# Kernel tuning notes

Measured on AMD Instinct MI355X. Metric: run time of the kernel, lower is better.

Reference implementation:

```python
import jax, jax.numpy as jnp
import numpy as np

BETA = 0.5      # conf.beta (undefined global in original repo)
ALPHA = 0.2     # LeakyReLU negative slope (init arg alpha)
N, E, FIN, FOUT = 50000, 1_600_000, 128, 64


def setup_inputs() -> dict:
    key = jax.random.key(0)
    k1, k2, k3, k4, k5 = jax.random.split(key, 5)
    inp = jax.random.normal(k1, (N, FIN), dtype=jnp.float32)
    edge = jax.random.randint(k2, (2, E), 0, N)                      # [2,E] (src,dst), = adj.nonzero().t()
    M_vals = jax.random.uniform(k3, (E,), dtype=jnp.float32)          # M gathered at edges
    # xavier_normal with gain 1.414, matching torch init
    W = jax.random.normal(k4, (FIN, FOUT), dtype=jnp.float32) * (1.414 * np.sqrt(2.0 / (FIN + FOUT)))
    a = jax.random.normal(k5, (2 * FOUT,), dtype=jnp.float32) * (1.414 * np.sqrt(2.0 / (1 + 2 * FOUT)))
    return {"input": inp, "M_vals": M_vals, "W": W, "a": a, "edge": edge}


def reference(input, M_vals, W, a, edge):
    n, f = input.shape[0], W.shape[1]
    src, dst = edge[0], edge[1]
    h = input @ W                                   # [N, F]
    # M = beta*M + (1-beta)*adj; at edges adj == 1
    bias = M_vals * BETA + (1.0 - BETA)             # [E]
    # a . cat(h_src, bias*h_dst) == (h@a[:F])[src] + bias * (h@a[F:])[dst]
    s1 = h @ a[:f]                                  # [N]
    s2 = h @ a[f:]                                  # [N]
    edge_e = jnp.exp(jax.nn.leaky_relu(s1[src] + bias * s2[dst], negative_slope=ALPHA))  # [E]
    # special_spmm(edge, e, [N,N], ones) -> per-row sum of edge weights
    e_rowsum = jax.ops.segment_sum(edge_e, src, num_segments=n)       # [N]
    # special_spmm(edge, e, [N,N], h) -> weighted aggregation of dst features into src rows
    h_prime = jax.ops.segment_sum(edge_e[:, None] * h[dst], src, num_segments=n)  # [N, F]
    h_prime = h_prime / e_rowsum[:, None]
    return jax.nn.elu(h_prime)                      # concat=True
```

## Files before the change

### kernel.cpp

```cpp
#include <hip/hip_runtime.h>
#include <hip/hip_bf16.h>

#define NN   50000
#define EE   1600000
#define FIN  128
#define FOUT 64
#define BETA  0.5f
#define ALPHA 0.2f
#define SBW    256
#define NB2    196
#define RCAP   9000
#define PGRID  400
#define PCHUNK 4000
#define CAP3   9008
#define XS     136

typedef __attribute__((ext_vector_type(8))) short short8;
typedef __attribute__((ext_vector_type(8))) unsigned short ushort8v;
typedef __attribute__((ext_vector_type(4))) float float4v;

__device__ __forceinline__ float load_any(const void* p, long i, int isf32) {
    if (isf32) return ((const float*)p)[i];
    unsigned int b = ((unsigned int)(((const unsigned short*)p)[i])) << 16;
    return __uint_as_float(b);
}

__device__ __forceinline__ unsigned short f32_to_bf16_rne(float f) {
    unsigned int b = __float_as_uint(f);
    return (unsigned short)((b + 0x7FFF + ((b >> 16) & 1)) >> 16);
}

__device__ __forceinline__ float bf16_to_f32(unsigned short u) {
    return __uint_as_float(((unsigned int)u) << 16);
}

__global__ __launch_bounds__(256) void detwt_kernel(
    const void* __restrict__ W, const void* __restrict__ Mv,
    unsigned short* __restrict__ Wt, int* __restrict__ flags,
    int* __restrict__ bcur)
{
    __shared__ int vote;
    const int tid = threadIdx.x;
    if (tid == 0) vote = 0;
    __syncthreads();

    int m = 0;
    const float vw = bf16_to_f32(((const unsigned short*)W)[tid * 16]);
    if (isnan(vw) || fabsf(vw) > 1e4f) m |= 1;
    if (blockIdx.x == 0) {
        const long half = (long)EE >> 1;
        const long pos = 2 * (((long)tid * (half / 256)) % half);
        const float vm = bf16_to_f32(((const unsigned short*)Mv)[pos]);
        if (isnan(vm) || fabsf(vm) > 1e4f) m |= 2;
    }
    if (m) atomicOr(&vote, m);
    __syncthreads();

    const int fW = vote & 1;
    if (blockIdx.x == 0) {
        if (tid == 0) flags[1] = (vote >> 1) & 1;
        if (tid < NB2) bcur[tid] = 0;
    }
    const int i = blockIdx.x * 256 + tid;
    const int k = i >> 6, n = i & 63;
    Wt[n * FIN + k] = f32_to_bf16_rne(load_any(W, i, fW));
}

__global__ __launch_bounds__(256) void mfma_gemm_kernel(
    const void* __restrict__ inp,
    const unsigned short* __restrict__ Wt,
    const void* __restrict__ a,
    unsigned short* __restrict__ h,
    float* __restrict__ s1,
    float* __restrict__ s2,
    int* __restrict__ flags)
{
    __shared__ unsigned short Xs[16 * XS];
    __shared__ float part1[4][16];
    __shared__ float part2[4][16];
    __shared__ int vote;

    const int tid  = threadIdx.x;
    const int wave = tid >> 6;
    const int lane = tid & 63;
    const int quad = lane >> 4;
    const int col  = lane & 15;
    const int rb   = blockIdx.x * 16;

    if (tid == 0) vote = 0;
    __syncthreads();

    {
        int m = 0;
        const float vi = bf16_to_f32(((const unsigned short*)inp)[(long)rb * FIN + tid * 8]);
        if (isnan(vi) || fabsf(vi) > 1e4f) m |= 1;
        if (tid < 128) {
            const float va = bf16_to_f32(((const unsigned short*)a)[tid]);
            if (isnan(va) || fabsf(va) > 1e4f) m |= 2;
        }
        if (m) atomicOr(&vote, m);
    }
    __syncthreads();
    const int fI = vote & 1, fA = (vote >> 1) & 1;
    if (blockIdx.x == 0 && tid == 0) flags[0] = fI;

    {
        const int r = tid >> 4, k8 = (tid & 15) * 8;
        if (!fI) {
            const unsigned short* src = (const unsigned short*)inp + (long)(rb + r) * FIN + k8;
            *(ushort8v*)&Xs[r * XS + k8] = *(const ushort8v*)src;
        } else {
            const float* src = (const float*)inp + (long)(rb + r) * FIN + k8;
            ushort8v v;
            #pragma unroll
            for (int j = 0; j < 8; ++j) v[j] = f32_to_bf16_rne(src[j]);
            *(ushort8v*)&Xs[r * XS + k8] = v;
        }
    }
    __syncthreads();

    const int nb = wave * 16;
    float4v acc = { 0.f, 0.f, 0.f, 0.f };
    #pragma unroll
    for (int k0 = 0; k0 < FIN; k0 += 32) {
        const short8 af = *(const short8*)&Xs[col * XS + k0 + quad * 8];
        const short8 bf = *(const short8*)&Wt[(long)(nb + col) * FIN + k0 + quad * 8];
        acc = __builtin_amdgcn_mfma_f32_16x16x32_bf16(af, bf, acc, 0, 0, 0);
    }

    #pragma unroll
    for (int r = 0; r < 4; ++r)
        h[(long)(rb + quad * 4 + r) * FOUT + nb + col] = f32_to_bf16_rne(acc[r]);

    const float a1 = load_any(a, nb + col, fA);
    const float a2 = load_any(a, 64 + nb + col, fA);
    #pragma unroll
    for (int r = 0; r < 4; ++r) {
        float v1 = acc[r] * a1;
        float v2 = acc[r] * a2;
        #pragma unroll
        for (int o = 1; o < 16; o <<= 1) {
            v1 += __shfl_xor(v1, o, 64);
            v2 += __shfl_xor(v2, o, 64);
        }
        if (col == 0) {
            part1[wave][quad * 4 + r] = v1;
            part2[wave][quad * 4 + r] = v2;
        }
    }
    __syncthreads();
    if (tid < 16) {
        s1[rb + tid] = part1[0][tid] + part1[1][tid] + part1[2][tid] + part1[3][tid];
        s2[rb + tid] = part2[0][tid] + part2[1][tid] + part2[2][tid] + part2[3][tid];
    }
}

__global__ __launch_bounds__(1024) void partition_kernel(
    const int* __restrict__ edge,
    const void* __restrict__ Mv,
    const int* __restrict__ flags,
    const float* __restrict__ s1,
    const float* __restrict__ s2,
    int* __restrict__ bcur,
    unsigned long long* __restrict__ recs)
{
    __shared__ int lcnt[NB2];
    __shared__ int lbase[NB2];
    const int tid = threadIdx.x;
    const int fM = flags[1];
    const int e0 = blockIdx.x * PCHUNK;

    if (tid < NB2) lcnt[tid] = 0;
    __syncthreads();

    int srcs[4], dsts[4];
    float mvs[4];
    #pragma unroll
    for (int k = 0; k < 4; ++k) {
        const int e = e0 + tid + 1024 * k;
        const bool ok = (tid + 1024 * k) < PCHUNK;
        srcs[k] = ok ? edge[e] : -1;
        dsts[k] = ok ? edge[EE + e] : 0;
        mvs[k]  = ok ? load_any(Mv, e, fM) : 0.f;
    }
    #pragma unroll
    for (int k = 0; k < 4; ++k)
        if (srcs[k] >= 0) atomicAdd(&lcnt[srcs[k] >> 8], 1);
    __syncthreads();

    if (tid < NB2) {
        const int c = lcnt[tid];
        const int o = c ? atomicAdd(&bcur[tid], c) : 0;
        lbase[tid] = tid * RCAP + o;
        lcnt[tid] = 0;
    }
    __syncthreads();

    float ss1[4], ss2[4];
    #pragma unroll
    for (int k = 0; k < 4; ++k) {
        ss1[k] = (srcs[k] >= 0) ? s1[srcs[k]] : 0.f;
        ss2[k] = (srcs[k] >= 0) ? s2[dsts[k]] : 0.f;
    }
    #pragma unroll
    for (int k = 0; k < 4; ++k) {
        if (srcs[k] < 0) continue;
        const float bias = mvs[k] * BETA + (1.f - BETA);
        const float x  = ss1[k] + bias * ss2[k];
        const float lr = x > 0.f ? x : ALPHA * x;
        const float ee = __expf(lr);
        const int b = srcs[k] >> 8;
        const int r = atomicAdd(&lcnt[b], 1);
        const int pos = lbase[b] + r;
        if (pos < (b + 1) * RCAP)
            recs[pos] = ((unsigned long long)(unsigned)srcs[k] << 32)
                      | ((unsigned long long)(unsigned)dsts[k] << 16)
                      | (unsigned long long)f32_to_bf16_rne(ee);
    }
}

__global__ __launch_bounds__(1024) void csr_spmm_kernel(
    const int* __restrict__ bcur,
    const unsigned long long* __restrict__ recs,
    const unsigned short* __restrict__ h,
    const int* __restrict__ flags,
    void* __restrict__ out)
{
    __shared__ unsigned long long lrec[CAP3];
    __shared__ unsigned int lpair[CAP3];
    __shared__ int cnt[SBW];
    __shared__ int off[SBW];
    __shared__ int wsum[4];
    const int b    = blockIdx.x;
    const int tid  = threadIdx.x;
    const int rb   = b * SBW;
    const int beg  = b * RCAP;

    int n = bcur[b]; if (n > RCAP) n = RCAP;

    if (tid < SBW) cnt[tid] = 0;
    __syncthreads();

    for (int j = tid; j < n; j += 1024) {
        const unsigned long long rec = recs[beg + j];
        const int r = (int)(rec >> 32) - rb;
        const int rank = atomicAdd(&cnt[r], 1);
        lrec[j] = ((unsigned long long)(unsigned)(r | (rank << 8)) << 32)
                | (unsigned long long)(unsigned)(rec & 0xFFFFFFFFu);
    }
    __syncthreads();

    int c = 0, x = 0;
    if (tid < SBW) {
        const int lane = tid & 63;
        c = cnt[tid];
        x = c;
        #pragma unroll
        for (int o = 1; o < 64; o <<= 1) {
            int y = __shfl_up(x, o, 64);
            if (lane >= o) x += y;
        }
        if (lane == 63) wsum[tid >> 6] = x;
    }
    __syncthreads();
    if (tid < SBW) {
        const int wv = tid >> 6;
        int wb = 0;
        for (int w = 0; w < wv; ++w) wb += wsum[w];
        off[tid] = wb + x - c;
    }
    __syncthreads();

    for (int j = tid; j < n; j += 1024) {
        const unsigned long long rec = lrec[j];
        const unsigned int hi = (unsigned int)(rec >> 32);
        lpair[off[hi & 255u] + (hi >> 8)] = (unsigned int)(rec & 0xFFFFFFFFu);
    }
    __syncthreads();

    const int wv   = tid >> 6;
    const int lane = tid & 63;
    const int g    = lane >> 3;
    const int sl   = lane & 7;
    const int fOut = flags[0];

    for (int rr = wv; rr < SBW; rr += 16) {
        const int row = rb + rr;
        if (row >= NN) break;
        const int jb = off[rr];
        const int je = jb + cnt[rr];

        float acc0 = 0.f, acc1 = 0.f, acc2 = 0.f, acc3 = 0.f;
        float acc4 = 0.f, acc5 = 0.f, acc6 = 0.f, acc7 = 0.f;
        float rsum = 0.f;
        int j = jb;
        for (; j + 31 < je; j += 32) {
            unsigned int u[4];
            #pragma unroll
            for (int kk = 0; kk < 4; ++kk) u[kk] = lpair[j + 8 * kk + g];
            ushort8v hv[4];
            #pragma unroll
            for (int kk = 0; kk < 4; ++kk)
                hv[kk] = *(const ushort8v*)&h[(long)(u[kk] >> 16) * FOUT + 8 * sl];
            #pragma unroll
            for (int kk = 0; kk < 4; ++kk) {
                const float v = bf16_to_f32((unsigned short)(u[kk] & 0xFFFFu));
                rsum += v;
                acc0 = fmaf(v, bf16_to_f32(hv[kk][0]), acc0);
                acc1 = fmaf(v, bf16_to_f32(hv[kk][1]), acc1);
                acc2 = fmaf(v, bf16_to_f32(hv[kk][2]), acc2);
                acc3 = fmaf(v, bf16_to_f32(hv[kk][3]), acc3);
                acc4 = fmaf(v, bf16_to_f32(hv[kk][4]), acc4);
                acc5 = fmaf(v, bf16_to_f32(hv[kk][5]), acc5);
                acc6 = fmaf(v, bf16_to_f32(hv[kk][6]), acc6);
                acc7 = fmaf(v, bf16_to_f32(hv[kk][7]), acc7);
            }
        }
        for (; j + 7 < je; j += 8) {
            const unsigned int u = lpair[j + g];
            const ushort8v hv = *(const ushort8v*)&h[(long)(u >> 16) * FOUT + 8 * sl];
            const float v = bf16_to_f32((unsigned short)(u & 0xFFFFu));
            rsum += v;
            acc0 = fmaf(v, bf16_to_f32(hv[0]), acc0);
            acc1 = fmaf(v, bf16_to_f32(hv[1]), acc1);
            acc2 = fmaf(v, bf16_to_f32(hv[2]), acc2);
            acc3 = fmaf(v, bf16_to_f32(hv[3]), acc3);
            acc4 = fmaf(v, bf16_to_f32(hv[4]), acc4);
            acc5 = fmaf(v, bf16_to_f32(hv[5]), acc5);
            acc6 = fmaf(v, bf16_to_f32(hv[6]), acc6);
            acc7 = fmaf(v, bf16_to_f32(hv[7]), acc7);
        }
        if (j < je && j + g < je) {
            const unsigned int u = lpair[j + g];
            const ushort8v hv = *(const ushort8v*)&h[(long)(u >> 16) * FOUT + 8 * sl];
            const float v = bf16_to_f32((unsigned short)(u & 0xFFFFu));
            rsum += v;
            acc0 = fmaf(v, bf16_to_f32(hv[0]), acc0);
            acc1 = fmaf(v, bf16_to_f32(hv[1]), acc1);
            acc2 = fmaf(v, bf16_to_f32(hv[2]), acc2);
            acc3 = fmaf(v, bf16_to_f32(hv[3]), acc3);
            acc4 = fmaf(v, bf16_to_f32(hv[4]), acc4);
            acc5 = fmaf(v, bf16_to_f32(hv[5]), acc5);
            acc6 = fmaf(v, bf16_to_f32(hv[6]), acc6);
            acc7 = fmaf(v, bf16_to_f32(hv[7]), acc7);
        }

        #pragma unroll
        for (int o = 8; o < 64; o <<= 1) {
            rsum += __shfl_xor(rsum, o, 64);
            acc0 += __shfl_xor(acc0, o, 64);
            acc1 += __shfl_xor(acc1, o, 64);
            acc2 += __shfl_xor(acc2, o, 64);
            acc3 += __shfl_xor(acc3, o, 64);
            acc4 += __shfl_xor(acc4, o, 64);
            acc5 += __shfl_xor(acc5, o, 64);
            acc6 += __shfl_xor(acc6, o, 64);
            acc7 += __shfl_xor(acc7, o, 64);
        }

        if (g == 0) {
            const float inv = 1.f / rsum;
            float q0 = acc0 * inv, q1 = acc1 * inv, q2 = acc2 * inv, q3 = acc3 * inv;
            float q4 = acc4 * inv, q5 = acc5 * inv, q6 = acc6 * inv, q7 = acc7 * inv;
            q0 = q0 > 0.f ? q0 : (__expf(q0) - 1.f);
            q1 = q1 > 0.f ? q1 : (__expf(q1) - 1.f);
            q2 = q2 > 0.f ? q2 : (__expf(q2) - 1.f);
            q3 = q3 > 0.f ? q3 : (__expf(q3) - 1.f);
            q4 = q4 > 0.f ? q4 : (__expf(q4) - 1.f);
            q5 = q5 > 0.f ? q5 : (__expf(q5) - 1.f);
            q6 = q6 > 0.f ? q6 : (__expf(q6) - 1.f);
            q7 = q7 > 0.f ? q7 : (__expf(q7) - 1.f);
            if (fOut) {
                float4* o = (float4*)((float*)out + (long)row * FOUT + 8 * sl);
                o[0] = make_float4(q0, q1, q2, q3);
                o[1] = make_float4(q4, q5, q6, q7);
            } else {
                ushort8v ov;
                ov[0] = f32_to_bf16_rne(q0); ov[1] = f32_to_bf16_rne(q1);
                ov[2] = f32_to_bf16_rne(q2); ov[3] = f32_to_bf16_rne(q3);
                ov[4] = f32_to_bf16_rne(q4); ov[5] = f32_to_bf16_rne(q5);
                ov[6] = f32_to_bf16_rne(q6); ov[7] = f32_to_bf16_rne(q7);
                *(ushort8v*)((unsigned short*)out + (long)row * FOUT + 8 * sl) = ov;
            }
        }
    }
}

extern "C" void kernel_launch(void* const* d_in, const int* in_sizes, int n_in,
                              void* d_out, int out_size, void* d_ws, size_t ws_size,
                              hipStream_t stream) {
    const void* inp  = d_in[0];
    const void* Mv   = d_in[1];
    const void* W    = d_in[2];
    const void* a    = d_in[3];
    const int*  edge = (const int*)d_in[4];

    char* p = (char*)d_ws;
    int*                flags  = (int*)p;            p += 256;
    unsigned short*     Wt     = (unsigned short*)p; p += ((size_t)FOUT * FIN * 2 + 255) / 256 * 256;
    unsigned short*     h      = (unsigned short*)p; p += ((size_t)NN * FOUT * 2 + 255) / 256 * 256;
    float*              s1     = (float*)p;          p += ((size_t)NN * 4 + 255) / 256 * 256;
    float*              s2     = (float*)p;          p += ((size_t)NN * 4 + 255) / 256 * 256;
    int*                bcur   = (int*)p;            p += ((size_t)NB2 * 4 + 255) / 256 * 256;
    unsigned long long* recs   = (unsigned long long*)p;

    detwt_kernel<<<32, 256, 0, stream>>>(W, Mv, Wt, flags, bcur);
    mfma_gemm_kernel<<<NN / 16, 256, 0, stream>>>(inp, Wt, a, h, s1, s2, flags);
    partition_kernel<<<PGRID, 1024, 0, stream>>>(edge, Mv, flags, s1, s2, bcur, recs);
    csr_spmm_kernel<<<NB2, 1024, 0, stream>>>(bcur, recs, h, flags, d_out);
}
```

Measured before the change: 174.5 us.

## Use 64-row buckets and one 8-lane group per row in SpMM

Shrinks the partition buckets from 256 to 64 source rows, giving 782 SpMM blocks of 512 threads instead of 196 blocks of 1024, so more CUs are busy and per-block LDS use drops. Each row is now handled by one 8-lane group that walks its own edge list sequentially, replacing whole-wave processing followed by cross-group shuffle reductions. The row-offset prefix scan collapses to a single-wave scan. Trade-offs: the partition kernel now does more global atomics on bucket counters, RCAP=2500 per bucket is a tighter cap that could silently drop edges for skewed inputs, and lanes in a wave see uneven work when row degrees differ.

```diff
diff --git a/kernel.cpp b/kernel.cpp
--- a/kernel.cpp
+++ b/kernel.cpp
@@ -7,12 +7,13 @@
 #define FOUT 64
 #define BETA  0.5f
 #define ALPHA 0.2f
-#define SBW    256
-#define NB2    196
-#define RCAP   9000
+#define SBW    64
+#define SBSH   6
+#define NB     782
+#define RCAP   2500
 #define PGRID  400
 #define PCHUNK 4000
-#define CAP3   9008
+#define CAPB   2504
 #define XS     136
 
 typedef __attribute__((ext_vector_type(8))) short short8;
@@ -59,7 +60,7 @@
     const int fW = vote & 1;
     if (blockIdx.x == 0) {
         if (tid == 0) flags[1] = (vote >> 1) & 1;
-        if (tid < NB2) bcur[tid] = 0;
+        for (int i = tid; i < NB; i += 256) bcur[i] = 0;
     }
     const int i = blockIdx.x * 256 + tid;
     const int k = i >> 6, n = i & 63;
@@ -164,13 +165,13 @@
     int* __restrict__ bcur,
     unsigned long long* __restrict__ recs)
 {
-    __shared__ int lcnt[NB2];
-    __shared__ int lbase[NB2];
+    __shared__ int lcnt[NB];
+    __shared__ int lbase[NB];
     const int tid = threadIdx.x;
     const int fM = flags[1];
     const int e0 = blockIdx.x * PCHUNK;
 
-    if (tid < NB2) lcnt[tid] = 0;
+    if (tid < NB) lcnt[tid] = 0;
     __syncthreads();
 
     int srcs[4], dsts[4];
@@ -185,10 +186,10 @@
     }
     #pragma unroll
     for (int k = 0; k < 4; ++k)
-        if (srcs[k] >= 0) atomicAdd(&lcnt[srcs[k] >> 8], 1);
-    __syncthreads();
-
-    if (tid < NB2) {
+        if (srcs[k] >= 0) atomicAdd(&lcnt[srcs[k] >> SBSH], 1);
+    __syncthreads();
+
+    if (tid < NB) {
         const int c = lcnt[tid];
         const int o = c ? atomicAdd(&bcur[tid], c) : 0;
         lbase[tid] = tid * RCAP + o;
@@ -209,7 +210,7 @@
         const float x  = ss1[k] + bias * ss2[k];
         const float lr = x > 0.f ? x : ALPHA * x;
         const float ee = __expf(lr);
-        const int b = srcs[k] >> 8;
+        const int b = srcs[k] >> SBSH;
         const int r = atomicAdd(&lcnt[b], 1);
         const int pos = lbase[b] + r;
         if (pos < (b + 1) * RCAP)
@@ -219,18 +220,17 @@
     }
 }
 
-__global__ __launch_bounds__(1024) void csr_spmm_kernel(
+__global__ __launch_bounds__(512) void csr_spmm_kernel(
     const int* __restrict__ bcur,
     const unsigned long long* __restrict__ recs,
     const unsigned short* __restrict__ h,
     const int* __restrict__ flags,
     void* __restrict__ out)
 {
-    __shared__ unsigned long long lrec[CAP3];
-    __shared__ unsigned int lpair[CAP3];
+    __shared__ unsigned long long lrec[CAPB];
+    __shared__ unsigned int lpair[CAPB];
     __shared__ int cnt[SBW];
     __shared__ int off[SBW];
-    __shared__ int wsum[4];
     const int b    = blockIdx.x;
     const int tid  = threadIdx.x;
     const int rb   = b * SBW;
@@ -241,7 +241,7 @@
     if (tid < SBW) cnt[tid] = 0;
     __syncthreads();
 
-    for (int j = tid; j < n; j += 1024) {
+    for (int j = tid; j < n; j += 512) {
         const unsigned long long rec = recs[beg + j];
         const int r = (int)(rec >> 32) - rb;
         const int rank = atomicAdd(&cnt[r], 1);
@@ -250,138 +250,109 @@
     }
     __syncthreads();
 
-    int c = 0, x = 0;
     if (tid < SBW) {
-        const int lane = tid & 63;
-        c = cnt[tid];
-        x = c;
-        #pragma unroll
-        for (int o = 1; o < 64; o <<= 1) {
+        const int c = cnt[tid];
+        int x = c;
+        #pragma unroll
+        for (int o = 1; o < SBW; o <<= 1) {
             int y = __shfl_up(x, o, 64);
-            if (lane >= o) x += y;
-        }
-        if (lane == 63) wsum[tid >> 6] = x;
-    }
-    __syncthreads();
-    if (tid < SBW) {
-        const int wv = tid >> 6;
-        int wb = 0;
-        for (int w = 0; w < wv; ++w) wb += wsum[w];
-        off[tid] = wb + x - c;
-    }
-    __syncthreads();
-
-    for (int j = tid; j < n; j += 1024) {
+            if (tid >= o) x += y;
+        }
+        off[tid] = x - c;
+    }
+    __syncthreads();
+
+    for (int j = tid; j < n; j += 512) {
         const unsigned long long rec = lrec[j];
         const unsigned int hi = (unsigned int)(rec >> 32);
-        lpair[off[hi & 255u] + (hi >> 8)] = (unsigned int)(rec & 0xFFFFFFFFu);
+        lpair[off[hi & 63u] + (hi >> 8)] = (unsigned int)(rec & 0xFFFFFFFFu);
     }
     __syncthreads();
 
     const int wv   = tid >> 6;
     const int lane = tid & 63;
-    const int g    = lane >> 3;
+    const int gr   = lane >> 3;
     const int sl   = lane & 7;
+    const int rr   = wv * 8 + gr;
+    const int row  = rb + rr;
     const int fOut = flags[0];
 
-    for (int rr = wv; rr < SBW; rr += 16) {
-        const int row = rb + rr;
-        if (row >= NN) break;
-        const int jb = off[rr];
-        const int je = jb + cnt[rr];
-
-        float acc0 = 0.f, acc1 = 0.f, acc2 = 0.f, acc3 = 0.f;
-        float acc4 = 0.f, acc5 = 0.f, acc6 = 0.f, acc7 = 0.f;
-        float rsum = 0.f;
-        int j = jb;
-        for (; j + 31 < je; j += 32) {
-            unsigned int u[4];
-            #pragma unroll
-            for (int kk = 0; kk < 4; ++kk) u[kk] = lpair[j + 8 * kk + g];
-            ushort8v hv[4];
-            #pragma unroll
-            for (int kk = 0; kk < 4; ++kk)
-                hv[kk] = *(const ushort8v*)&h[(long)(u[kk] >> 16) * FOUT + 8 * sl];
-            #pragma unroll
-            for (int kk = 0; kk < 4; ++kk) {
-                const float v = bf16_to_f32((unsigned short)(u[kk] & 0xFFFFu));
-                rsum += v;
-                acc0 = fmaf(v, bf16_to_f32(hv[kk][0]), acc0);
-                acc1 = fmaf(v, bf16_to_f32(hv[kk][1]), acc1);
-                acc2 = fmaf(v, bf16_to_f32(hv[kk][2]), acc2);
-                acc3 = fmaf(v, bf16_to_f32(hv[kk][3]), acc3);
-                acc4 = fmaf(v, bf16_to_f32(hv[kk][4]), acc4);
-                acc5 = fmaf(v, bf16_to_f32(hv[kk][5]), acc5);
-                acc6 = fmaf(v, bf16_to_f32(hv[kk][6]), acc6);
-                acc7 = fmaf(v, bf16_to_f32(hv[kk][7]), acc7);
-            }
-        }
-        for (; j + 7 < je; j += 8) {
-            const unsigned int u = lpair[j + g];
-            const ushort8v hv = *(const ushort8v*)&h[(long)(u >> 16) * FOUT + 8 * sl];
-            const float v = bf16_to_f32((unsigned short)(u & 0xFFFFu));
+    const int jb = off[rr];
+    const int je = jb + cnt[rr];
+
+    float acc0 = 0.f, acc1 = 0.f, acc2 = 0.f, acc3 = 0.f;
+    float acc4 = 0.f, acc5 = 0.f, acc6 = 0.f, acc7 = 0.f;
+    float rsum = 0.f;
+    int j = jb;
+    for (; j + 3 < je; j += 4) {
+        unsigned int u[4];
+        #pragma unroll
+        for (int kk = 0; kk < 4; ++kk) u[kk] = lpair[j + kk];
+        ushort8v hv[4];
+        #pragma unroll
+        for (int kk = 0; kk < 4; ++kk)
+            hv[kk] = *(const ushort8v*)&h[(long)(u[kk] >> 16) * FOUT + 8 * sl];
+        #pragma unroll
+        for (int kk = 0; kk < 4; ++kk) {
+            const float v = bf16_to_f32((unsigned short)(u[kk] & 0xFFFFu));
             rsum += v;
-            acc0 = fmaf(v, bf16_to_f32(hv[0]), acc0);
-            acc1 = fmaf(v, bf16_to_f32(hv[1]), acc1);
-            acc2 = fmaf(v, bf16_to_f32(hv[2]), acc2);
-            acc3 = fmaf(v, bf16_to_f32(hv[3]), acc3);
-            acc4 = fmaf(v, bf16_to_f32(hv[4]), acc4);
-            acc5 = fmaf(v, bf16_to_f32(hv[5]), acc5);
-            acc6 = fmaf(v, bf16_to_f32(hv[6]), acc6);
-            acc7 = fmaf(v, bf16_to_f32(hv[7]), acc7);
-        }
-        if (j < je && j + g < je) {
-            const unsigned int u = lpair[j + g];
-            const ushort8v hv = *(const ushort8v*)&h[(long)(u >> 16) * FOUT + 8 * sl];
-            const float v = bf16_to_f32((unsigned short)(u & 0xFFFFu));
-            rsum += v;
-            acc0 = fmaf(v, bf16_to_f32(hv[0]), acc0);
-            acc1 = fmaf(v, bf16_to_f32(hv[1]), acc1);
-            acc2 = fmaf(v, bf16_to_f32(hv[2]), acc2);
-            acc3 = fmaf(v, bf16_to_f32(hv[3]), acc3);
-            acc4 = fmaf(v, bf16_to_f32(hv[4]), acc4);
-            acc5 = fmaf(v, bf16_to_f32(hv[5]), acc5);
-            acc6 = fmaf(v, bf16_to_f32(hv[6]), acc6);
-            acc7 = fmaf(v, bf16_to_f32(hv[7]), acc7);
-        }
-
-        #pragma unroll
-        for (int o = 8; o < 64; o <<= 1) {
-            rsum += __shfl_xor(rsum, o, 64);
-            acc0 += __shfl_xor(acc0, o, 64);
-            acc1 += __shfl_xor(acc1, o, 64);
-            acc2 += __shfl_xor(acc2, o, 64);
-            acc3 += __shfl_xor(acc3, o, 64);
-            acc4 += __shfl_xor(acc4, o, 64);
-            acc5 += __shfl_xor(acc5, o, 64);
-            acc6 += __shfl_xor(acc6, o, 64);
-            acc7 += __shfl_xor(acc7, o, 64);
-        }
-
-        if (g == 0) {
-            const float inv = 1.f / rsum;
-            float q0 = acc0 * inv, q1 = acc1 * inv, q2 = acc2 * inv, q3 = acc3 * inv;
-            float q4 = acc4 * inv, q5 = acc5 * inv, q6 = acc6 * inv, q7 = acc7 * inv;
-            q0 = q0 > 0.f ? q0 : (__expf(q0) - 1.f);
-            q1 = q1 > 0.f ? q1 : (__expf(q1) - 1.f);
-            q2 = q2 > 0.f ? q2 : (__expf(q2) - 1.f);
-            q3 = q3 > 0.f ? q3 : (__expf(q3) - 1.f);
-            q4 = q4 > 0.f ? q4 : (__expf(q4) - 1.f);
-            q5 = q5 > 0.f ? q5 : (__expf(q5) - 1.f);
-            q6 = q6 > 0.f ? q6 : (__expf(q6) - 1.f);
-            q7 = q7 > 0.f ? q7 : (__expf(q7) - 1.f);
-            if (fOut) {
-                float4* o = (float4*)((float*)out + (long)row * FOUT + 8 * sl);
-                o[0] = make_float4(q0, q1, q2, q3);
-                o[1] = make_float4(q4, q5, q6, q7);
-            } else {
-                ushort8v ov;
-                ov[0] = f32_to_bf16_rne(q0); ov[1] = f32_to_bf16_rne(q1);
-                ov[2] = f32_to_bf16_rne(q2); ov[3] = f32_to_bf16_rne(q3);
-                ov[4] = f32_to_bf16_rne(q4); ov[5] = f32_to_bf16_rne(q5);
-                ov[6] = f32_to_bf16_rne(q6); ov[7] = f32_to_bf16_rne(q7);
-                *(ushort8v*)((unsigned short*)out + (long)row * FOUT + 8 * sl) = ov;
-            }
+            acc0 = fmaf(v, bf16_to_f32(hv[kk][0]), acc0);
+            acc1 = fmaf(v, bf16_to_f32(hv[kk][1]), acc1);
+            acc2 = fmaf(v, bf16_to_f32(hv[kk][2]), acc2);
+            acc3 = fmaf(v, bf16_to_f32(hv[kk][3]), acc3);
+            acc4 = fmaf(v, bf16_to_f32(hv[kk][4]), acc4);
+            acc5 = fmaf(v, bf16_to_f32(hv[kk][5]), acc5);
+            acc6 = fmaf(v, bf16_to_f32(hv[kk][6]), acc6);
+            acc7 = fmaf(v, bf16_to_f32(hv[kk][7]), acc7);
+        }
+    }
+    for (; j < je; ++j) {
+        const unsigned int u = lpair[j];
+        const ushort8v hv = *(const ushort8v*)&h[(long)(u >> 16) * FOUT + 8 * sl];
+        const float v = bf16_to_f32((unsigned short)(u & 0xFFFFu));
+        rsum += v;
+        acc0 = fmaf(v, bf16_to_f32(hv[0]), acc0);
+        acc1 = fmaf(v, bf16_to_f32(hv[1]), acc1);
+        acc2 = fmaf(v, bf16_to_f32(hv[2]), acc2);
+        acc3 = fmaf(v, bf16_to_f32(hv[3]), acc3);
+        acc4 = fmaf(v, bf16_to_f32(hv[4]), acc4);
+        acc5 = fmaf(v, bf16_to_f32(hv[5]), acc5);
+        acc6 = fmaf(v, bf16_to_f32(hv[6]), acc6);
+        acc7 = fmaf(v, bf16_to_f32(hv[7]), acc7);
+    }
+
+    if (row < NN && je > jb) {
+        const float inv = 1.f / rsum;
+        float q0 = acc0 * inv, q1 = acc1 * inv, q2 = acc2 * inv, q3 = acc3 * inv;
+        float q4 = acc4 * inv, q5 = acc5 * inv, q6 = acc6 * inv, q7 = acc7 * inv;
+        q0 = q0 > 0.f ? q0 : (__expf(q0) - 1.f);
+        q1 = q1 > 0.f ? q1 : (__expf(q1) - 1.f);
+        q2 = q2 > 0.f ? q2 : (__expf(q2) - 1.f);
+        q3 = q3 > 0.f ? q3 : (__expf(q3) - 1.f);
+        q4 = q4 > 0.f ? q4 : (__expf(q4) - 1.f);
+        q5 = q5 > 0.f ? q5 : (__expf(q5) - 1.f);
+        q6 = q6 > 0.f ? q6 : (__expf(q6) - 1.f);
+        q7 = q7 > 0.f ? q7 : (__expf(q7) - 1.f);
+        if (fOut) {
+            float4* o = (float4*)((float*)out + (long)row * FOUT + 8 * sl);
+            o[0] = make_float4(q0, q1, q2, q3);
+            o[1] = make_float4(q4, q5, q6, q7);
+        } else {
+            ushort8v ov;
+            ov[0] = f32_to_bf16_rne(q0); ov[1] = f32_to_bf16_rne(q1);
+            ov[2] = f32_to_bf16_rne(q2); ov[3] = f32_to_bf16_rne(q3);
+            ov[4] = f32_to_bf16_rne(q4); ov[5] = f32_to_bf16_rne(q5);
+            ov[6] = f32_to_bf16_rne(q6); ov[7] = f32_to_bf16_rne(q7);
+            *(ushort8v*)((unsigned short*)out + (long)row * FOUT + 8 * sl) = ov;
+        }
+    } else if (row < NN) {
+        if (fOut) {
+            float4* o = (float4*)((float*)out + (long)row * FOUT + 8 * sl);
+            o[0] = make_float4(0.f, 0.f, 0.f, 0.f);
+            o[1] = make_float4(0.f, 0.f, 0.f, 0.f);
+        } else {
+            ushort8v ov = { 0, 0, 0, 0, 0, 0, 0, 0 };
+            *(ushort8v*)((unsigned short*)out + (long)row * FOUT + 8 * sl) = ov;
         }
     }
 }
@@ -401,11 +372,11 @@
     unsigned short*     h      = (unsigned short*)p; p += ((size_t)NN * FOUT * 2 + 255) / 256 * 256;
     float*              s1     = (float*)p;          p += ((size_t)NN * 4 + 255) / 256 * 256;
     float*              s2     = (float*)p;          p += ((size_t)NN * 4 + 255) / 256 * 256;
-    int*                bcur   = (int*)p;            p += ((size_t)NB2 * 4 + 255) / 256 * 256;
+    int*                bcur   = (int*)p;            p += ((size_t)NB * 4 + 255) / 256 * 256;
     unsigned long long* recs   = (unsigned long long*)p;
 
     detwt_kernel<<<32, 256, 0, stream>>>(W, Mv, Wt, flags, bcur);
     mfma_gemm_kernel<<<NN / 16, 256, 0, stream>>>(inp, Wt, a, h, s1, s2, flags);
     partition_kernel<<<PGRID, 1024, 0, stream>>>(edge, Mv, flags, s1, s2, bcur, recs);
-    csr_spmm_kernel<<<NB2, 1024, 0, stream>>>(bcur, recs, h, flags, d_out);
-}
+    csr_spmm_kernel<<<NB, 512, 0, stream>>>(bcur, recs, h, flags, d_out);
+}
```

After: 155.3 us. -11.0%, faster.
